# Kernel tuning notes

Hardware: AMD Instinct MI355X
Metric: run time of the kernel (lower is better)

The kernel has to match this reference:

```python
import jax, jax.numpy as jnp
import numpy as np

N, L, I, H, D = 8192, 8, 256, 512, 8
PER = N // D  # nodes per depth level; level 0 nodes are tree roots


def setup_inputs() -> dict:
    key = jax.random.key(0)
    ks = jax.random.split(key, 9)
    s = 0.05
    x_seq = jax.random.normal(ks[0], (N, L, I), jnp.float32)
    # GRU params (torch nn.GRU layout, gate order r,z,n), stored transposed [in, 3H]
    W_ih = jax.random.normal(ks[1], (I, 3 * H), jnp.float32) * s
    W_hh = jax.random.normal(ks[2], (H, 3 * H), jnp.float32) * s
    b_ih = jax.random.normal(ks[3], (3 * H,), jnp.float32) * s
    b_hh = jax.random.normal(ks[4], (3 * H,), jnp.float32) * s
    # Child-sum TreeLSTM params: x-projections for i,o,u,f and recurrent U's
    Wx = jax.random.normal(ks[5], (H, 4 * H), jnp.float32) * s
    bx = jax.random.normal(ks[6], (4 * H,), jnp.float32) * s
    U_iou = jax.random.normal(ks[7], (H, 3 * H), jnp.float32) * s
    U_f = jax.random.normal(ks[8], (H, H), jnp.float32) * s
    # Forest structure: D levels of PER nodes; node at level d>0 has a random
    # parent at level d-1; roots (level 0) point at themselves (contribution is
    # zero because their own state is still zero when level 0 is processed).
    rng = np.random.default_rng(0)
    depth = np.repeat(np.arange(D), PER).astype(np.int32)
    parent = np.arange(N, dtype=np.int32)
    for d in range(1, D):
        parent[d * PER:(d + 1) * PER] = rng.integers((d - 1) * PER, d * PER, PER)
    root_ids = np.arange(PER, dtype=np.int32)
    return {
        "x_seq": x_seq, "W_ih": W_ih, "W_hh": W_hh, "b_ih": b_ih, "b_hh": b_hh,
        "Wx": Wx, "bx": bx, "U_iou": U_iou, "U_f": U_f,
        "parent": jnp.asarray(parent), "depth": jnp.asarray(depth),
        "root_ids": jnp.asarray(root_ids), "n_levels": D,
    }


def reference(x_seq, W_ih, W_hh, b_ih, b_hh, Wx, bx, U_iou, U_f,
              parent, depth, root_ids, n_levels):
    n = x_seq.shape[0]
    h_dim = W_hh.shape[0]

    # --- GRU over each node's encoding sequence (all nodes batched) ---
    def gru_step(h, x_t):  # h: [N,H], x_t: [N,I]
        gi = x_t @ W_ih + b_ih
        gh = h @ W_hh + b_hh
        ir, iz, inn = jnp.split(gi, 3, axis=-1)
        hr, hz, hn = jnp.split(gh, 3, axis=-1)
        r = jax.nn.sigmoid(ir + hr)
        z = jax.nn.sigmoid(iz + hz)
        ng = jnp.tanh(inn + r * hn)
        return (1.0 - z) * ng + z * h, None

    h0 = jnp.zeros((n, h_dim), x_seq.dtype)
    enc, _ = jax.lax.scan(gru_step, h0, jnp.swapaxes(x_seq, 0, 1))  # [N,H]

    # --- Child-sum TreeLSTM, processed leaves -> roots by depth level ---
    xg = enc @ Wx + bx  # [N,4H]
    xi, xo, xu, xf = jnp.split(xg, 4, axis=-1)
    c = jnp.zeros((n, h_dim), x_seq.dtype)
    h = jnp.zeros((n, h_dim), x_seq.dtype)
    for level in range(n_levels - 1, -1, -1):
        h_sum = jax.ops.segment_sum(h, parent, num_segments=n)  # sum over children
        giou = h_sum @ U_iou
        i = jax.nn.sigmoid(xi + giou[:, :h_dim])
        o = jax.nn.sigmoid(xo + giou[:, h_dim:2 * h_dim])
        u = jnp.tanh(xu + giou[:, 2 * h_dim:])
        # per-child forget gate uses parent's x projection and child's h
        f = jax.nn.sigmoid(xf[parent] + h @ U_f)
        fc = jax.ops.segment_sum(f * c, parent, num_segments=n)
        c_new = i * u + fc
        mask = (depth == level)[:, None]
        c = jnp.where(mask, c_new, c)
        h = jnp.where(mask, o * jnp.tanh(c_new), h)

    # root states per tree, stacked as [2, n_trees, H] -> (c_root, h_root)
    return jnp.stack([c[root_ids], h[root_ids]])
```

## Files before the change

kernel.cpp:

```cpp
#include <hip/hip_runtime.h>
#include <math.h>

typedef short bf16x8 __attribute__((ext_vector_type(8)));
typedef float f32x4 __attribute__((ext_vector_type(4)));

__device__ __forceinline__ float sigf(float x) {
    return __builtin_amdgcn_rcpf(1.f + __expf(-x));
}
__device__ __forceinline__ float tanhf_fast(float x) {
    const float e = __expf(2.f * x);
    return 1.f - 2.f * __builtin_amdgcn_rcpf(e + 1.f);
}

__device__ __forceinline__ unsigned short f2bf(float f) {
    union { float f; unsigned u; } v; v.f = f;
    unsigned r = (v.u + 0x7FFFu + ((v.u >> 16) & 1u)) >> 16;
    return (unsigned short)r;
}
__device__ __forceinline__ float bf2f(unsigned short u) {
    union { unsigned u; float f; } v; v.u = ((unsigned)u) << 16; return v.f;
}

__device__ __forceinline__ void gload16(const unsigned short* g, unsigned short* l) {
    __builtin_amdgcn_global_load_lds(
        (const __attribute__((address_space(1))) void*)g,
        (__attribute__((address_space(3))) void*)l, 16, 0, 0);
}

__device__ __forceinline__ int swz(int slot, int row) {
    return (slot ^ ((row >> 1) & 3)) * 8;
}
__device__ __forceinline__ int tix(int ml, int jl) {
    return ((ml >> 4) * 2 + (jl >> 5)) * 512 + (ml & 15) * 32 + (jl & 31);
}

__global__ void cvt_f32_bf16(const float* __restrict__ src,
                             unsigned short* __restrict__ dst, int n)
{
    const int i = (blockIdx.x * blockDim.x + threadIdx.x) * 4;
    if (i >= n) return;
    const float4 v = *reinterpret_cast<const float4*>(src + i);
    ushort4 o;
    o.x = f2bf(v.x); o.y = f2bf(v.y); o.z = f2bf(v.z); o.w = f2bf(v.w);
    *reinterpret_cast<ushort4*>(dst + i) = o;
}

__global__ void transpose_cvt(const float* __restrict__ src,
                              unsigned short* __restrict__ dst,
                              int rows, int cols)
{
    __shared__ float tile[32][33];
    const int bc = blockIdx.x * 32, br = blockIdx.y * 32;
    const int tx = threadIdx.x, ty = threadIdx.y;
    #pragma unroll
    for (int i = 0; i < 32; i += 8)
        tile[ty + i][tx] = src[(size_t)(br + ty + i) * cols + bc + tx];
    __syncthreads();
    #pragma unroll
    for (int i = 0; i < 32; i += 8)
        dst[(size_t)(bc + ty + i) * rows + br + tx] = f2bf(tile[tx][ty + i]);
}

__global__ __launch_bounds__(256)
void gemm_bf16out(const unsigned short* __restrict__ A,
                  const unsigned short* __restrict__ BT,
                  const float* __restrict__ bias,
                  unsigned short* __restrict__ Cb, int M, int N, int K,
                  int ncols)
{
    const int nwg = (int)gridDim.x;
    const int l = ((int)blockIdx.x & 7) * (nwg >> 3) + ((int)blockIdx.x >> 3);
    const int m0 = (l / ncols) * 128, n0 = (l % ncols) * 128;
    const int tid = (int)threadIdx.x, lane = tid & 63, wid = tid >> 6;
    const int wm = wid >> 1, wn = wid & 1;
    const int fr = lane & 15, kg = lane >> 4;
    const int lrow = lane >> 2;
    const int scol = swz(lane & 3, lrow);

    __shared__ unsigned short smem[3 * 8192];

    f32x4 acc[4][4];
    #pragma unroll
    for (int i = 0; i < 4; ++i)
        #pragma unroll
        for (int j = 0; j < 4; ++j)
            acc[i][j] = (f32x4){0.f, 0.f, 0.f, 0.f};

    auto stage = [&](int buf, int kt) {
        const int k0 = kt * 32;
        unsigned short* base = &smem[buf * 8192];
        #pragma unroll
        for (int q = 0; q < 4; ++q) {
            const int c = wid * 4 + q;
            const unsigned short* g = (c < 8)
                ? A + (size_t)(m0 + c * 16 + lrow) * K + k0 + scol
                : BT + (size_t)(n0 + (c - 8) * 16 + lrow) * K + k0 + scol;
            gload16(g, base + c * 512);
        }
    };

    const int nkt = K >> 5;
    stage(0, 0); stage(1, 1); stage(2, 2);
    int cur = 0;

    for (int kt = 0; kt < nkt; ++kt) {
        if (kt + 2 < nkt)      asm volatile("s_waitcnt vmcnt(8)" ::: "memory");
        else if (kt + 1 < nkt) asm volatile("s_waitcnt vmcnt(4)" ::: "memory");
        else                   asm volatile("s_waitcnt vmcnt(0)" ::: "memory");
        __builtin_amdgcn_s_barrier();

        const unsigned short* sb = &smem[cur * 8192];
        bf16x8 af[4], bf[4];
        #pragma unroll
        for (int mi = 0; mi < 4; ++mi) {
            const int row = wm * 64 + mi * 16 + fr;
            af[mi] = *reinterpret_cast<const bf16x8*>(&sb[row * 32 + swz(kg, row)]);
        }
        #pragma unroll
        for (int ni = 0; ni < 4; ++ni) {
            const int row = wn * 64 + ni * 16 + fr;
            bf[ni] = *reinterpret_cast<const bf16x8*>(&sb[4096 + row * 32 + swz(kg, row)]);
        }
        asm volatile("s_waitcnt lgkmcnt(0)" ::: "memory");
        __builtin_amdgcn_s_barrier();
        if (kt + 3 < nkt) stage(cur, kt + 3);

        __builtin_amdgcn_s_setprio(1);
        #pragma unroll
        for (int mi = 0; mi < 4; ++mi)
            #pragma unroll
            for (int ni = 0; ni < 4; ++ni)
                acc[mi][ni] = __builtin_amdgcn_mfma_f32_16x16x32_bf16(
                    af[mi], bf[ni], acc[mi][ni], 0, 0, 0);
        __builtin_amdgcn_s_setprio(0);
        cur = (cur == 2) ? 0 : cur + 1;
    }

    #pragma unroll
    for (int ni = 0; ni < 4; ++ni) {
        const int nl = wn * 64 + ni * 16 + fr;
        const float bv = bias[n0 + nl];
        #pragma unroll
        for (int mi = 0; mi < 4; ++mi)
            #pragma unroll
            for (int r = 0; r < 4; ++r) {
                const int ml = wm * 64 + mi * 16 + kg * 4 + r;
                smem[ml * 132 + nl] = f2bf(acc[mi][ni][r] + bv);
            }
    }
    __syncthreads();
    #pragma unroll
    for (int e = 0; e < 8; ++e) {
        const int id = tid + e * 256;
        const int row = id >> 4, cw = id & 15;
        const int4 v = *reinterpret_cast<const int4*>(&smem[row * 132 + cw * 8]);
        *reinterpret_cast<int4*>(&Cb[(size_t)(m0 + row) * N + n0 + cw * 8]) = v;
    }
}

__global__ void gru_step0(const unsigned short* __restrict__ gi,
                          unsigned short* __restrict__ hbo,
                          const float* __restrict__ b_hh)
{
    constexpr int H = 512, G3H = 1536, L = 8;
    const int idx = blockIdx.x * blockDim.x + threadIdx.x;
    const int m = idx >> 6, jv = idx & 63;
    const size_t gb = (size_t)m * L * G3H + jv * 8;
    const bf16x8 gr8 = *reinterpret_cast<const bf16x8*>(gi + gb);
    const bf16x8 gz8 = *reinterpret_cast<const bf16x8*>(gi + gb + H);
    const bf16x8 gn8 = *reinterpret_cast<const bf16x8*>(gi + gb + 2 * H);
    bf16x8 o;
    #pragma unroll
    for (int k = 0; k < 8; ++k) {
        const int j = jv * 8 + k;
        const float r = sigf(bf2f((unsigned short)gr8[k]) + b_hh[j]);
        const float z = sigf(bf2f((unsigned short)gz8[k]) + b_hh[H + j]);
        const float n = tanhf_fast(bf2f((unsigned short)gn8[k]) + r * b_hh[2 * H + j]);
        o[k] = (short)f2bf((1.f - z) * n);
    }
    *reinterpret_cast<bf16x8*>(hbo + (size_t)m * H + jv * 8) = o;
}

__global__ __launch_bounds__(256, 3)
void gru_step(const unsigned short* __restrict__ gi,
              int t,
              const unsigned short* __restrict__ hbi,
              unsigned short* __restrict__ hbo,
              const unsigned short* __restrict__ WhhT,
              const float* __restrict__ b_hh)
{
    constexpr int H = 512, G3H = 1536, L = 8;
    const int m0 = blockIdx.x * 64, j0 = blockIdx.y * 64;
    const int tid = (int)threadIdx.x, lane = tid & 63, wid = tid >> 6;
    const int wm = wid >> 1, wn = wid & 1;
    const int fr = lane & 15, kg = lane >> 4;
    const int lrow = lane >> 2;
    const int scol = swz(lane & 3, lrow);
    const int ucol = (lane & 3) * 8;

    __shared__ unsigned short smem[3 * 8192];

    f32x4 ar[2][2], az[2][2], ah[2][2];
    #pragma unroll
    for (int i = 0; i < 2; ++i)
        #pragma unroll
        for (int j = 0; j < 2; ++j) {
            ar[i][j] = (f32x4){0.f, 0.f, 0.f, 0.f};
            az[i][j] = (f32x4){0.f, 0.f, 0.f, 0.f};
            ah[i][j] = (f32x4){0.f, 0.f, 0.f, 0.f};
        }

    constexpr int nkt = H / 32;

    auto stage = [&](int buf, int kt) {
        const int k0 = kt * 32;
        unsigned short* base = &smem[buf * 8192];
        #pragma unroll
        for (int q = 0; q < 4; ++q) {
            const int c = wid * 4 + q;
            if (c < 4) {
                const unsigned short* g =
                    hbi + (size_t)(m0 + c * 16 + lrow) * H + k0 + scol;
                gload16(g, base + c * 512);
            } else {
                const int gate = (c - 4) >> 2, rowg = (c - 4) & 3;
                const unsigned short* g =
                    WhhT + (size_t)(gate * H + j0 + rowg * 16 + lrow) * H + k0 + scol;
                gload16(g, base + c * 512);
            }
        }
    };
    auto stage_epi = [&](int ep) {
        unsigned short* base = &smem[(ep + 1) * 8192];
        #pragma unroll
        for (int q = 0; q < 4; ++q) {
            const int c = wid * 4 + q;
            const int part = c >> 3, cc = c & 7;
            const int rowg = cc >> 1, colg = cc & 1;
            const unsigned short* src;
            if (ep == 0)
                src = gi + ((size_t)(m0 + rowg * 16 + lrow) * L + t) * G3H
                         + part * H + j0 + colg * 32 + ucol;
            else if (part == 0)
                src = gi + ((size_t)(m0 + rowg * 16 + lrow) * L + t) * G3H
                         + 2 * H + j0 + colg * 32 + ucol;
            else
                src = hbi + (size_t)(m0 + rowg * 16 + lrow) * H
                          + j0 + colg * 32 + ucol;
            gload16(src, base + part * 4096 + cc * 512);
        }
    };

    stage(0, 0); stage(1, 1); stage(2, 2);
    int cur = 0;

    for (int kt = 0; kt < nkt; ++kt) {
        asm volatile("s_waitcnt vmcnt(8)" ::: "memory");
        __builtin_amdgcn_s_barrier();

        const unsigned short* sb = &smem[cur * 8192];
        bf16x8 af[2], bfr[2], bfz[2], bfn[2];
        #pragma unroll
        for (int mi = 0; mi < 2; ++mi) {
            const int row = wm * 32 + mi * 16 + fr;
            af[mi] = *reinterpret_cast<const bf16x8*>(&sb[row * 32 + swz(kg, row)]);
        }
        #pragma unroll
        for (int ni = 0; ni < 2; ++ni) {
            const int row = wn * 32 + ni * 16 + fr;
            const int sw = swz(kg, row);
            bfr[ni] = *reinterpret_cast<const bf16x8*>(&sb[2048 + (row) * 32 + sw]);
            bfz[ni] = *reinterpret_cast<const bf16x8*>(&sb[2048 + (64 + row) * 32 + sw]);
            bfn[ni] = *reinterpret_cast<const bf16x8*>(&sb[2048 + (128 + row) * 32 + sw]);
        }
        asm volatile("s_waitcnt lgkmcnt(0)" ::: "memory");
        __builtin_amdgcn_s_barrier();
        if (kt + 3 < nkt)       stage(cur, kt + 3);
        else if (kt == nkt - 3) stage_epi(0);
        else if (kt == nkt - 2) stage_epi(1);

        __builtin_amdgcn_s_setprio(1);
        #pragma unroll
        for (int mi = 0; mi < 2; ++mi)
            #pragma unroll
            for (int ni = 0; ni < 2; ++ni) {
                ar[mi][ni] = __builtin_amdgcn_mfma_f32_16x16x32_bf16(af[mi], bfr[ni], ar[mi][ni], 0, 0, 0);
                az[mi][ni] = __builtin_amdgcn_mfma_f32_16x16x32_bf16(af[mi], bfz[ni], az[mi][ni], 0, 0, 0);
                ah[mi][ni] = __builtin_amdgcn_mfma_f32_16x16x32_bf16(af[mi], bfn[ni], ah[mi][ni], 0, 0, 0);
            }
        __builtin_amdgcn_s_setprio(0);
        cur = (cur == 2) ? 0 : cur + 1;
    }

    asm volatile("s_waitcnt vmcnt(0)" ::: "memory");
    __builtin_amdgcn_s_barrier();

    unsigned short res[2][2][4];
    #pragma unroll
    for (int ni = 0; ni < 2; ++ni) {
        const int jl = wn * 32 + ni * 16 + fr;
        const int j = j0 + jl;
        const float bhr = b_hh[j], bhz = b_hh[H + j], bhn = b_hh[2 * H + j];
        #pragma unroll
        for (int mi = 0; mi < 2; ++mi) {
            #pragma unroll
            for (int r = 0; r < 4; ++r) {
                const int ml = wm * 32 + mi * 16 + kg * 4 + r;
                const int ix = tix(ml, jl);
                const float gr = bf2f(smem[8192 + ix]);
                const float gz = bf2f(smem[12288 + ix]);
                const float gn = bf2f(smem[16384 + ix]);
                const float hv = bf2f(smem[20480 + ix]);
                const float rg = sigf(ar[mi][ni][r] + gr + bhr);
                const float zg = sigf(az[mi][ni][r] + gz + bhz);
                const float ng = tanhf_fast(gn + rg * (ah[mi][ni][r] + bhn));
                res[ni][mi][r] = f2bf((1.f - zg) * ng + zg * hv);
            }
        }
    }

    #pragma unroll
    for (int ni = 0; ni < 2; ++ni) {
        const int jl = wn * 32 + ni * 16 + fr;
        #pragma unroll
        for (int mi = 0; mi < 2; ++mi)
            #pragma unroll
            for (int r = 0; r < 4; ++r) {
                const int ml = wm * 32 + mi * 16 + kg * 4 + r;
                smem[tix(ml, jl)] = res[ni][mi][r];
            }
    }
    __syncthreads();

    #pragma unroll
    for (int e = 0; e < 2; ++e) {
        const int id = tid + e * 256;
        const int ml = id >> 3, jw = id & 7;
        const int4 v = *reinterpret_cast<const int4*>(
            &smem[((ml >> 4) * 2 + (jw >> 2)) * 512 + (ml & 15) * 32 + (jw & 3) * 8]);
        *reinterpret_cast<int4*>(&hbo[(size_t)(m0 + ml) * H + j0 + jw * 8]) = v;
    }
}

__global__ __launch_bounds__(256, 4)
void tree_gemm(const unsigned short* __restrict__ hTb,
               const unsigned short* __restrict__ UcombT,
               const unsigned short* __restrict__ xgb,
               const float* __restrict__ cT,
               const int* __restrict__ parent,
               int cstart, int pstart,
               float* __restrict__ giou,
               float* __restrict__ fcs)
{
    constexpr int H = 512, N4H = 2048, G3H = 1536;
    const int nwg = (int)gridDim.x;
    const int l = ((int)blockIdx.x & 7) * (nwg >> 3) + ((int)blockIdx.x >> 3);
    const int m0 = (l >> 5) * 64, n0 = (l & 31) * 64;
    const int tid = (int)threadIdx.x, lane = tid & 63, wid = tid >> 6;
    const int wm = wid >> 1, wn = wid & 1;
    const int fr = lane & 15, kg = lane >> 4;
    const int lrow = lane >> 2;
    const int scol = swz(lane & 3, lrow);

    __shared__ unsigned short smem[4 * 4096];

    f32x4 acc[2][2];
    #pragma unroll
    for (int i = 0; i < 2; ++i)
        #pragma unroll
        for (int j = 0; j < 2; ++j)
            acc[i][j] = (f32x4){0.f, 0.f, 0.f, 0.f};

    auto stage = [&](int buf, int kt) {
        const int k0 = kt * 32;
        unsigned short* base = &smem[buf * 4096];
        #pragma unroll
        for (int q = 0; q < 2; ++q) {
            const int c = wid * 2 + q;
            const unsigned short* g = (c < 4)
                ? hTb + (size_t)(cstart + m0 + c * 16 + lrow) * H + k0 + scol
                : UcombT + (size_t)(n0 + (c - 4) * 16 + lrow) * H + k0 + scol;
            gload16(g, base + c * 512);
        }
    };

    constexpr int nkt = H / 32;
    stage(0, 0); stage(1, 1); stage(2, 2); stage(3, 3);
    int cur = 0;

    for (int kt = 0; kt < nkt; ++kt) {
        if (kt + 3 < nkt)      asm volatile("s_waitcnt vmcnt(6)" ::: "memory");
        else if (kt + 2 < nkt) asm volatile("s_waitcnt vmcnt(4)" ::: "memory");
        else if (kt + 1 < nkt) asm volatile("s_waitcnt vmcnt(2)" ::: "memory");
        else                   asm volatile("s_waitcnt vmcnt(0)" ::: "memory");
        __builtin_amdgcn_s_barrier();

        const unsigned short* sb = &smem[cur * 4096];
        bf16x8 af[2], bf[2];
        #pragma unroll
        for (int mi = 0; mi < 2; ++mi) {
            const int row = wm * 32 + mi * 16 + fr;
            af[mi] = *reinterpret_cast<const bf16x8*>(&sb[row * 32 + swz(kg, row)]);
        }
        #pragma unroll
        for (int ni = 0; ni < 2; ++ni) {
            const int row = wn * 32 + ni * 16 + fr;
            bf[ni] = *reinterpret_cast<const bf16x8*>(&sb[2048 + row * 32 + swz(kg, row)]);
        }
        asm volatile("s_waitcnt lgkmcnt(0)" ::: "memory");
        __builtin_amdgcn_s_barrier();
        if (kt + 4 < nkt) stage(cur, kt + 4);

        __builtin_amdgcn_s_setprio(1);
        #pragma unroll
        for (int mi = 0; mi < 2; ++mi)
            #pragma unroll
            for (int ni = 0; ni < 2; ++ni)
                acc[mi][ni] = __builtin_amdgcn_mfma_f32_16x16x32_bf16(
                    af[mi], bf[ni], acc[mi][ni], 0, 0, 0);
        __builtin_amdgcn_s_setprio(0);
        cur = (cur == 3) ? 0 : cur + 1;
    }

    if (n0 < G3H) {
        #pragma unroll
        for (int mi = 0; mi < 2; ++mi)
            #pragma unroll
            for (int r = 0; r < 4; ++r) {
                const int m = m0 + wm * 32 + mi * 16 + kg * 4 + r;
                const int p = parent[cstart + m] - pstart;
                #pragma unroll
                for (int ni = 0; ni < 2; ++ni) {
                    const int n = n0 + wn * 32 + ni * 16 + fr;
                    atomicAdd(&giou[(size_t)p * G3H + n], acc[mi][ni][r]);
                }
            }
    } else {
        #pragma unroll
        for (int mi = 0; mi < 2; ++mi)
            #pragma unroll
            for (int r = 0; r < 4; ++r) {
                const int m = m0 + wm * 32 + mi * 16 + kg * 4 + r;
                const int child = cstart + m;
                const int p = parent[child];
                #pragma unroll
                for (int ni = 0; ni < 2; ++ni) {
                    const int jf = n0 + wn * 32 + ni * 16 + fr - G3H;
                    const float f = sigf(acc[mi][ni][r] +
                                         bf2f(xgb[(size_t)p * N4H + G3H + jf]));
                    atomicAdd(&fcs[(size_t)(p - pstart) * H + jf],
                              f * cT[(size_t)child * H + jf]);
                }
            }
    }
}

__global__ void level_update(const unsigned short* __restrict__ xgb,
                             float* __restrict__ giou,
                             float* __restrict__ fcs,
                             float* __restrict__ cT, float* __restrict__ hT,
                             unsigned short* __restrict__ hb, int pstart,
                             float* __restrict__ outp, int PH)
{
    constexpr int H = 512, N4H = 2048, G3H = 1536;
    const int idx = blockIdx.x * blockDim.x + threadIdx.x;
    const int pi = idx >> 9, j = idx & (H - 1);
    const int p = pstart + pi;
    const size_t xb4 = (size_t)p * N4H;
    const size_t gb = (size_t)pi * G3H;
    const float ig = sigf(bf2f(xgb[xb4 + j]) + giou[gb + j]);
    const float og = sigf(bf2f(xgb[xb4 + H + j]) + giou[gb + H + j]);
    const float ug = tanhf_fast(bf2f(xgb[xb4 + 2 * H + j]) + giou[gb + 2 * H + j]);
    const float cn = ig * ug + fcs[idx];
    const float hn = og * tanhf_fast(cn);
    if (outp) {
        outp[idx] = cn;
        outp[(size_t)PH + idx] = hn;
    } else {
        const size_t off = (size_t)p * H + j;
        cT[off] = cn;
        hT[off] = hn;
        hb[off] = f2bf(hn);
        giou[gb + j] = 0.f;
        giou[gb + H + j] = 0.f;
        giou[gb + 2 * H + j] = 0.f;
        fcs[idx] = 0.f;
    }
}

extern "C" void kernel_launch(void* const* d_in, const int* in_sizes, int n_in,
                              void* d_out, int out_size, void* d_ws, size_t ws_size,
                              hipStream_t stream)
{
    const float* x_seq = (const float*)d_in[0];
    const float* W_ih  = (const float*)d_in[1];
    const float* W_hh  = (const float*)d_in[2];
    const float* b_ih  = (const float*)d_in[3];
    const float* b_hh  = (const float*)d_in[4];
    const float* Wx    = (const float*)d_in[5];
    const float* bx    = (const float*)d_in[6];
    const float* U_iou = (const float*)d_in[7];
    const float* U_f   = (const float*)d_in[8];
    const int* parent  = (const int*)d_in[9];

    const int threeH = in_sizes[3];
    const int H   = threeH / 3;
    const int I   = in_sizes[1] / threeH;
    const int N   = in_sizes[9];
    const int L   = in_sizes[0] / (N * I);
    const int PER = in_sizes[11];
    const int D   = N / PER;

    const size_t NH = (size_t)N * H;
    const size_t PH = (size_t)PER * H;

    char* p = (char*)d_ws;
    const size_t xb_sz  = (size_t)N * L * I * 2;
    const size_t xgb_sz = (size_t)N * 4 * H * 2;
    const size_t zone_sz = xb_sz > xgb_sz ? xb_sz : xgb_sz;
    unsigned short* xb  = (unsigned short*)p;
    unsigned short* xgb = (unsigned short*)p;    p += zone_sz;
    unsigned short* gi  = (unsigned short*)p;    p += (size_t)N * L * threeH * 2;
    unsigned short* hb0 = (unsigned short*)p;    p += NH * 2;
    unsigned short* hb1 = (unsigned short*)p;    p += NH * 2;
    unsigned short* WihT = (unsigned short*)p;   p += (size_t)threeH * I * 2;
    unsigned short* WhhT = (unsigned short*)p;   p += (size_t)threeH * H * 2;
    unsigned short* WxT  = (unsigned short*)p;   p += (size_t)4 * H * H * 2;
    unsigned short* UcombT = (unsigned short*)p; p += (size_t)4 * H * H * 2;
    if ((size_t)(p - (char*)d_ws) > ws_size) return;
    float* cT   = (float*)gi;
    float* hT   = cT + NH;
    float* giou = hT + NH;
    float* fcs  = giou + PH * 3;

    {
        const int n = N * L * I;
        cvt_f32_bf16<<<(n / 4 + 255) / 256, 256, 0, stream>>>(x_seq, xb, n);
        dim3 blk(32, 8);
        transpose_cvt<<<dim3(threeH / 32, I / 32), blk, 0, stream>>>(W_ih, WihT, I, threeH);
        transpose_cvt<<<dim3(threeH / 32, H / 32), blk, 0, stream>>>(W_hh, WhhT, H, threeH);
        transpose_cvt<<<dim3(4 * H / 32, H / 32), blk, 0, stream>>>(Wx, WxT, H, 4 * H);
        transpose_cvt<<<dim3(threeH / 32, H / 32), blk, 0, stream>>>(U_iou, UcombT, H, threeH);
        transpose_cvt<<<dim3(H / 32, H / 32), blk, 0, stream>>>(
            U_f, UcombT + (size_t)threeH * H, H, H);
    }

    gemm_bf16out<<<(N * L / 128) * (threeH / 128), 256, 0, stream>>>(
        xb, WihT, b_ih, gi, N * L, threeH, I, threeH / 128);

    gru_step0<<<(int)(NH / 8 / 256), 256, 0, stream>>>(gi, hb1, b_hh);
    {
        dim3 grid(N / 64, H / 64);
        for (int t = 1; t < L; ++t) {
            const unsigned short* hin = (t & 1) ? hb1 : hb0;
            unsigned short* hout = (t & 1) ? hb0 : hb1;
            gru_step<<<grid, 256, 0, stream>>>(gi, t, hin, hout, WhhT, b_hh);
        }
    }

    gemm_bf16out<<<(N / 128) * (4 * H / 128), 256, 0, stream>>>(
        hb0, WxT, bx, xgb, N, 4 * H, H, 4 * H / 128);

    hipMemsetAsync(giou, 0, PH * 4 * 4, stream);
    unsigned short* hTb = hb1;
    const int pw_blocks = (int)(PH / 256);

    for (int lvl = D - 1; lvl >= 0; --lvl) {
        const int pstart = lvl * PER;
        const int cstart = (lvl + 1) * PER;

        if (lvl < D - 1)
            tree_gemm<<<(PER / 64) * (4 * H / 64), 256, 0, stream>>>(
                hTb, UcombT, xgb, cT, parent, cstart, pstart, giou, fcs);

        level_update<<<pw_blocks, 256, 0, stream>>>(
            xgb, giou, fcs, cT, hT, hTb, pstart,
            (lvl == 0) ? (float*)d_out : nullptr, (int)PH);
    }
}
```

Baseline: 473.0 us.

## Store GRU input projections time-major and use nontemporal GEMM output stores

The input-projection GEMM now reads x with strided row addressing so its output is laid out time-major ([L][N][3H]). Each GRU step then reads one contiguous slab per timestep instead of rows strided by L*3H. The GEMM epilogue also switches to nontemporal stores. The layout change is meant to improve locality of the per-step gi loads, but the strided A reads in the GEMM are less contiguous, and nontemporal stores may hurt when the data is reread soon after.

Result: slower. 486.7 us (+2.9%).

```diff
diff --git a/kernel.cpp b/kernel.cpp
--- a/kernel.cpp
+++ b/kernel.cpp
@@ -3,6 +3,7 @@
 
 typedef short bf16x8 __attribute__((ext_vector_type(8)));
 typedef float f32x4 __attribute__((ext_vector_type(4)));
+typedef int i32x4 __attribute__((ext_vector_type(4)));
 
 __device__ __forceinline__ float sigf(float x) {
     return __builtin_amdgcn_rcpf(1.f + __expf(-x));
@@ -66,11 +67,13 @@
                   const unsigned short* __restrict__ BT,
                   const float* __restrict__ bias,
                   unsigned short* __restrict__ Cb, int M, int N, int K,
-                  int ncols)
+                  int ncols, int Mrows, int rstride, int tstride)
 {
     const int nwg = (int)gridDim.x;
     const int l = ((int)blockIdx.x & 7) * (nwg >> 3) + ((int)blockIdx.x >> 3);
     const int m0 = (l / ncols) * 128, n0 = (l % ncols) * 128;
+    const size_t abase = (size_t)(m0 % Mrows) * rstride
+                       + (size_t)(m0 / Mrows) * tstride;
     const int tid = (int)threadIdx.x, lane = tid & 63, wid = tid >> 6;
     const int wm = wid >> 1, wn = wid & 1;
     const int fr = lane & 15, kg = lane >> 4;
@@ -93,7 +96,7 @@
         for (int q = 0; q < 4; ++q) {
             const int c = wid * 4 + q;
             const unsigned short* g = (c < 8)
-                ? A + (size_t)(m0 + c * 16 + lrow) * K + k0 + scol
+                ? A + abase + (size_t)(c * 16 + lrow) * rstride + k0 + scol
                 : BT + (size_t)(n0 + (c - 8) * 16 + lrow) * K + k0 + scol;
             gload16(g, base + c * 512);
         }
@@ -153,8 +156,9 @@
     for (int e = 0; e < 8; ++e) {
         const int id = tid + e * 256;
         const int row = id >> 4, cw = id & 15;
-        const int4 v = *reinterpret_cast<const int4*>(&smem[row * 132 + cw * 8]);
-        *reinterpret_cast<int4*>(&Cb[(size_t)(m0 + row) * N + n0 + cw * 8]) = v;
+        const i32x4 v = *reinterpret_cast<const i32x4*>(&smem[row * 132 + cw * 8]);
+        __builtin_nontemporal_store(v,
+            reinterpret_cast<i32x4*>(&Cb[(size_t)(m0 + row) * N + n0 + cw * 8]));
     }
 }
 
@@ -162,10 +166,10 @@
                           unsigned short* __restrict__ hbo,
                           const float* __restrict__ b_hh)
 {
-    constexpr int H = 512, G3H = 1536, L = 8;
+    constexpr int H = 512, G3H = 1536;
     const int idx = blockIdx.x * blockDim.x + threadIdx.x;
     const int m = idx >> 6, jv = idx & 63;
-    const size_t gb = (size_t)m * L * G3H + jv * 8;
+    const size_t gb = (size_t)m * G3H + jv * 8;
     const bf16x8 gr8 = *reinterpret_cast<const bf16x8*>(gi + gb);
     const bf16x8 gz8 = *reinterpret_cast<const bf16x8*>(gi + gb + H);
     const bf16x8 gn8 = *reinterpret_cast<const bf16x8*>(gi + gb + 2 * H);
@@ -182,14 +186,13 @@
 }
 
 __global__ __launch_bounds__(256, 3)
-void gru_step(const unsigned short* __restrict__ gi,
-              int t,
+void gru_step(const unsigned short* __restrict__ giT,
               const unsigned short* __restrict__ hbi,
               unsigned short* __restrict__ hbo,
               const unsigned short* __restrict__ WhhT,
               const float* __restrict__ b_hh)
 {
-    constexpr int H = 512, G3H = 1536, L = 8;
+    constexpr int H = 512, G3H = 1536;
     const int m0 = blockIdx.x * 64, j0 = blockIdx.y * 64;
     const int tid = (int)threadIdx.x, lane = tid & 63, wid = tid >> 6;
     const int wm = wid >> 1, wn = wid & 1;
@@ -239,11 +242,11 @@
             const int rowg = cc >> 1, colg = cc & 1;
             const unsigned short* src;
             if (ep == 0)
-                src = gi + ((size_t)(m0 + rowg * 16 + lrow) * L + t) * G3H
-                         + part * H + j0 + colg * 32 + ucol;
+                src = giT + (size_t)(m0 + rowg * 16 + lrow) * G3H
+                          + part * H + j0 + colg * 32 + ucol;
             else if (part == 0)
-                src = gi + ((size_t)(m0 + rowg * 16 + lrow) * L + t) * G3H
-                         + 2 * H + j0 + colg * 32 + ucol;
+                src = giT + (size_t)(m0 + rowg * 16 + lrow) * G3H
+                          + 2 * H + j0 + colg * 32 + ucol;
             else
                 src = hbi + (size_t)(m0 + rowg * 16 + lrow) * H
                           + j0 + colg * 32 + ucol;
@@ -513,6 +516,7 @@
 
     const size_t NH = (size_t)N * H;
     const size_t PH = (size_t)PER * H;
+    const size_t NG = (size_t)N * threeH;
 
     char* p = (char*)d_ws;
     const size_t xb_sz  = (size_t)N * L * I * 2;
@@ -546,7 +550,8 @@
     }
 
     gemm_bf16out<<<(N * L / 128) * (threeH / 128), 256, 0, stream>>>(
-        xb, WihT, b_ih, gi, N * L, threeH, I, threeH / 128);
+        xb, WihT, b_ih, gi, N * L, threeH, I, threeH / 128,
+        N, L * I, I);
 
     gru_step0<<<(int)(NH / 8 / 256), 256, 0, stream>>>(gi, hb1, b_hh);
     {
@@ -554,12 +559,14 @@
         for (int t = 1; t < L; ++t) {
             const unsigned short* hin = (t & 1) ? hb1 : hb0;
             unsigned short* hout = (t & 1) ? hb0 : hb1;
-            gru_step<<<grid, 256, 0, stream>>>(gi, t, hin, hout, WhhT, b_hh);
+            gru_step<<<grid, 256, 0, stream>>>(gi + (size_t)t * NG, hin, hout,
+                                               WhhT, b_hh);
         }
     }
 
     gemm_bf16out<<<(N / 128) * (4 * H / 128), 256, 0, stream>>>(
-        hb0, WxT, bx, xgb, N, 4 * H, H, 4 * H / 128);
+        hb0, WxT, bx, xgb, N, 4 * H, H, 4 * H / 128,
+        N, H, 0);
 
     hipMemsetAsync(giou, 0, PH * 4 * 4, stream);
     unsigned short* hTb = hb1;
```
